# Kernel optimization log

Hardware: AMD Instinct MI355X
Metric: run time of the kernel (lower is better)

The kernel has to match this reference:

```python
import jax, jax.numpy as jnp
import numpy as np
import math
from itertools import combinations_with_replacement

M_MODES = 10      # photonic modes
N_PHOT = 5        # photons in input state [1,0,1,0,...]
HIDDEN = 100      # number of px phase shifters (hidden_dim)
IN_DIM = 784
N_CLASSES = 10
BATCH = 128

# Fock output states with bunching: multisets of N_PHOT modes -> C(14,5)=2002
_STATES = np.array(list(combinations_with_replacement(range(M_MODES), N_PHOT)), dtype=np.int32)  # [S, n] row indices
_FACT = np.array([
    np.prod([math.factorial(int(c)) for c in np.bincount(s, minlength=M_MODES)])
    for s in _STATES
], dtype=np.float32)  # prod t_j! per output state
# Input-state mode columns (occupied modes) and factorial product (=1 since all occupancies are 1)
_IN_COLS = np.array([0, 2, 4, 6, 8], dtype=np.int32)
# Ryser subsets over n=5 rows
_BITS = np.array([[(k >> i) & 1 for i in range(N_PHOT)] for k in range(2 ** N_PHOT)], dtype=np.float32)  # [K, n]
_SIGNS = ((-1.0) ** (N_PHOT - _BITS.sum(axis=1))).astype(np.float32)  # (-1)^n * (-1)^{|S|}


def _rand_unitary(rng, m):
    z = rng.standard_normal((m, m)) + 1j * rng.standard_normal((m, m))
    q, r = np.linalg.qr(z)
    q = q * (np.diag(r) / np.abs(np.diag(r)))
    return q.astype(np.complex64)


def setup_inputs() -> dict:
    rng = np.random.default_rng(0)
    x = jnp.asarray(rng.standard_normal((BATCH, IN_DIM)), dtype=jnp.float32)
    W1 = jnp.asarray(rng.standard_normal((HIDDEN, IN_DIM)) * 0.03, dtype=jnp.float32)
    b1 = jnp.zeros((HIDDEN,), dtype=jnp.float32)
    UL = _rand_unitary(rng, M_MODES)
    UR = _rand_unitary(rng, M_MODES)
    S = _STATES.shape[0]
    W2 = jnp.asarray(rng.standard_normal((N_CLASSES, S)) * 0.02, dtype=jnp.float32)
    b2 = jnp.zeros((N_CLASSES,), dtype=jnp.float32)
    return {
        "x": x, "W1": W1, "b1": b1,
        "wl_re": jnp.asarray(UL.real), "wl_im": jnp.asarray(UL.imag),
        "wr_re": jnp.asarray(UR.real), "wr_im": jnp.asarray(UR.imag),
        "W2": W2, "b2": b2,
    }


def _forward(x, W1, b1, wl_re, wl_im, wr_re, wr_im, W2, b2):
    B = x.shape[0]
    # downscaling linear + sigmoid -> phase-shifter values px in (0,1)
    h = jax.nn.sigmoid(x @ W1.T + b1)  # [B, HIDDEN]
    # phase shifter i sits on mode i % m; commuting phases on a mode sum
    theta = h.reshape(B, HIDDEN // M_MODES, M_MODES).sum(axis=1)  # [B, m]
    WL = (wl_re + 1j * wl_im).astype(jnp.complex64)
    WR = (wr_re + 1j * wr_im).astype(jnp.complex64)
    phase = jnp.exp(1j * theta.astype(jnp.complex64))  # [B, m]
    # total unitary U = WR @ diag(phase) @ WL
    U = jnp.einsum('pq,bq,qr->bpr', WR, phase, WL)  # [B, m, m]
    A = U[:, :, _IN_COLS]  # columns for occupied input modes -> [B, m, n]
    # per output Fock state, take rows (with multiplicity) -> [B, S, n, n]
    Mx = A[:, jnp.asarray(_STATES), :]
    masks = jnp.asarray(_BITS)   # [K, n]
    signs = jnp.asarray(_SIGNS)  # [K]
    # Ryser: perm = (-1)^n sum_S (-1)^{|S|} prod_j (sum_{i in S} M[i,j])
    rs = jnp.einsum('kn,bsnj->bskj', masks, Mx)       # [B, S, K, n]
    p = jnp.prod(rs, axis=-1)                          # [B, S, K]
    perm = jnp.einsum('k,bsk->bs', signs, p)           # [B, S] complex
    amp = perm / jnp.sqrt(jnp.asarray(_FACT))
    prob = amp.real ** 2 + amp.imag ** 2               # boson-sampling output distribution [B, S]
    return prob @ W2.T + b2                            # output Linear [B, N_CLASSES]


def reference(x, W1, b1, wl_re, wl_im, wr_re, wr_im, W2, b2):
    return _forward(x, W1, b1, wl_re, wl_im, wr_re, wr_im, W2, b2)
```

## Files before the change

### kernel.cpp

```cpp
#include <hip/hip_runtime.h>
#include <utility>
#include <math.h>

#define BATCH     128
#define IN_DIM    784
#define HIDDEN    100
#define MM        10
#define NPH       5
#define NSTATES   2002
#define NCLASSES  10

struct StateTbl { unsigned v[NSTATES]; };

constexpr StateTbl make_state_tbl() {
    StateTbl t{};
    int idx = 0;
    for (int a = 0; a < MM; ++a)
    for (int b = a; b < MM; ++b)
    for (int c = b; c < MM; ++c)
    for (int d = c; d < MM; ++d)
    for (int e = d; e < MM; ++e) {
        int cnt[MM] = {};
        cnt[a]++; cnt[b]++; cnt[c]++; cnt[d]++; cnt[e]++;
        int f = 1;
        for (int m = 0; m < MM; ++m) {
            int kf = 1;
            for (int i = 2; i <= cnt[m]; ++i) kf *= i;
            f *= kf;
        }
        t.v[idx++] = (unsigned)a | ((unsigned)b << 4) | ((unsigned)c << 8) |
                     ((unsigned)d << 12) | ((unsigned)e << 16) |
                     ((unsigned)f << 20);
    }
    return t;
}

__device__ const StateTbl STATE_TBL = make_state_tbl();

__global__ __launch_bounds__(256) void qc_stageA(
    const float* __restrict__ x, const float* __restrict__ W1,
    const float* __restrict__ b1,
    const float* __restrict__ wl_re, const float* __restrict__ wl_im,
    const float* __restrict__ wr_re, const float* __restrict__ wr_im,
    const float* __restrict__ b2,
    float* __restrict__ A_ws, float* __restrict__ out)
{
    __shared__ __align__(16) float xs[IN_DIM];
    __shared__ float part[200];
    __shared__ float hs[HIDDEN];
    __shared__ float phc[MM], phs_[MM];
    __shared__ float plr[50], pli[50];

    const int b   = blockIdx.x;
    const int tid = threadIdx.x;

    for (int i = tid; i < IN_DIM; i += 256) xs[i] = x[b * IN_DIM + i];
    if (tid < NCLASSES) out[b * NCLASSES + tid] = b2[tid];
    __syncthreads();

    if (tid < 200) {
        const int j = tid >> 1, half = tid & 1;
        const float* wr_ = W1 + j * IN_DIM + half * 392;
        const float* xr  = xs + half * 392;
        float4 acc = make_float4(0.f, 0.f, 0.f, 0.f);
        #pragma unroll 4
        for (int i = 0; i < 392; i += 4) {
            float4 w  = *(const float4*)(wr_ + i);
            float4 xv = *(const float4*)(xr + i);
            acc.x += w.x * xv.x; acc.y += w.y * xv.y;
            acc.z += w.z * xv.z; acc.w += w.w * xv.w;
        }
        part[tid] = (acc.x + acc.y) + (acc.z + acc.w);
    }
    __syncthreads();

    if (tid < HIDDEN) {
        float t = part[2 * tid] + part[2 * tid + 1] + b1[tid];
        hs[tid] = 1.0f / (1.0f + expf(-t));
    }
    __syncthreads();

    if (tid < MM) {
        float th = 0.f;
        #pragma unroll
        for (int g = 0; g < MM; ++g) th += hs[g * MM + tid];
        float sv, cv;
        sincosf(th, &sv, &cv);
        phc[tid] = cv; phs_[tid] = sv;
    }
    __syncthreads();

    if (tid < 50) {
        const int q = tid / 5, c = tid % 5;
        const float lr = wl_re[q * MM + 2 * c], li = wl_im[q * MM + 2 * c];
        plr[tid] = phc[q] * lr - phs_[q] * li;
        pli[tid] = phc[q] * li + phs_[q] * lr;
    }
    __syncthreads();

    if (tid < 50) {
        const int p = tid / 5, c = tid % 5;
        float ar = 0.f, ai = 0.f;
        #pragma unroll
        for (int q = 0; q < MM; ++q) {
            const float rr = wr_re[p * MM + q], ri = wr_im[p * MM + q];
            const float br = plr[q * 5 + c],    bi = pli[q * 5 + c];
            ar += rr * br - ri * bi;
            ai += rr * bi + ri * br;
        }
        A_ws[(b * 50 + tid) * 2 + 0] = ar;
        A_ws[(b * 50 + tid) * 2 + 1] = ai;
    }
}

template <int K>
__device__ __forceinline__ void ryser_step(
    const float (&mr)[5][5], const float (&mi)[5][5],
    float (&cr)[5], float (&ci)[5], float& accr, float& acci)
{
    constexpr int  bit  = (K & 1) ? 0 : ((K & 2) ? 1 : ((K & 4) ? 2 : ((K & 8) ? 3 : 4)));
    constexpr int  gray = K ^ (K >> 1);
    constexpr bool addf = ((gray >> bit) & 1) != 0;
    constexpr int  pc   = ((gray) & 1) + ((gray >> 1) & 1) + ((gray >> 2) & 1) +
                          ((gray >> 3) & 1) + ((gray >> 4) & 1);
    #pragma unroll
    for (int j = 0; j < 5; ++j) {
        if (addf) { cr[j] += mr[bit][j]; ci[j] += mi[bit][j]; }
        else      { cr[j] -= mr[bit][j]; ci[j] -= mi[bit][j]; }
    }
    float pr = cr[0], pi = ci[0];
    #pragma unroll
    for (int j = 1; j < 5; ++j) {
        const float nr = pr * cr[j] - pi * ci[j];
        const float ni = pr * ci[j] + pi * cr[j];
        pr = nr; pi = ni;
    }
    if constexpr (((NPH - pc) & 1) != 0) { accr -= pr; acci -= pi; }
    else                                 { accr += pr; acci += pi; }
}

template <int... Ks>
__device__ __forceinline__ void ryser_run(
    std::integer_sequence<int, Ks...>,
    const float (&mr)[5][5], const float (&mi)[5][5],
    float (&cr)[5], float (&ci)[5], float& accr, float& acci)
{
    (ryser_step<Ks + 1>(mr, mi, cr, ci, accr, acci), ...);
}

__global__ __launch_bounds__(256) void qc_stageB(
    const float* __restrict__ A_ws, const float* __restrict__ W2,
    float* __restrict__ out)
{
    __shared__ float2 a2[50];
    __shared__ float  wsum[4][NCLASSES];

    const int tid = threadIdx.x;
    const int b   = blockIdx.x >> 3;
    const int s   = ((blockIdx.x & 7) << 8) + tid;

    if (tid < 50) a2[tid] = ((const float2*)A_ws)[b * 50 + tid];
    __syncthreads();

    const bool valid = (s < NSTATES);
    float prob = 0.f;

    if (valid) {
        const unsigned w = STATE_TBL.v[s];

        float mr[5][5], mi[5][5];
        #pragma unroll
        for (int n = 0; n < 5; ++n) {
            const int base = ((w >> (4 * n)) & 15) * 5;
            #pragma unroll
            for (int j = 0; j < 5; ++j) {
                const float2 e = a2[base + j];
                mr[n][j] = e.x; mi[n][j] = e.y;
            }
        }

        float cr[5] = {0,0,0,0,0}, ci[5] = {0,0,0,0,0};
        float accr = 0.f, acci = 0.f;
        ryser_run(std::make_integer_sequence<int, 31>{}, mr, mi, cr, ci, accr, acci);

        const float fact = (float)(w >> 20);
        prob = (accr * accr + acci * acci) / fact;
    }

    #pragma unroll
    for (int c = 0; c < NCLASSES; ++c) {
        float v = 0.f;
        if (valid) v = prob * W2[c * NSTATES + s];
        #pragma unroll
        for (int off = 32; off > 0; off >>= 1) v += __shfl_down(v, off, 64);
        if ((tid & 63) == 0) wsum[tid >> 6][c] = v;
    }
    __syncthreads();
    if (tid < NCLASSES) {
        const float t = (wsum[0][tid] + wsum[1][tid]) + (wsum[2][tid] + wsum[3][tid]);
        atomicAdd(out + b * NCLASSES + tid, t);
    }
}

extern "C" void kernel_launch(void* const* d_in, const int* in_sizes, int n_in,
                              void* d_out, int out_size, void* d_ws, size_t ws_size,
                              hipStream_t stream)
{
    const float* x     = (const float*)d_in[0];
    const float* W1    = (const float*)d_in[1];
    const float* b1    = (const float*)d_in[2];
    const float* wl_re = (const float*)d_in[3];
    const float* wl_im = (const float*)d_in[4];
    const float* wr_re = (const float*)d_in[5];
    const float* wr_im = (const float*)d_in[6];
    const float* W2    = (const float*)d_in[7];
    const float* b2    = (const float*)d_in[8];
    float*       out   = (float*)d_out;
    float*       A_ws  = (float*)d_ws;

    qc_stageA<<<BATCH, 256, 0, stream>>>(x, W1, b1, wl_re, wl_im,
                                         wr_re, wr_im, b2, A_ws, out);
    qc_stageB<<<BATCH * 8, 256, 0, stream>>>(A_ws, W2, out);
}
```

Measured before the change: 101.0 us.

## Switch permanent computation from Ryser to Glynn Gray-code formula, two states per thread

New measurement: 95.47 us. 5.5% less time.

```diff
diff --git a/kernel.cpp b/kernel.cpp
--- a/kernel.cpp
+++ b/kernel.cpp
@@ -114,19 +114,20 @@
 }
 
 template <int K>
-__device__ __forceinline__ void ryser_step(
+__device__ __forceinline__ void glynn_step(
     const float (&mr)[5][5], const float (&mi)[5][5],
     float (&cr)[5], float (&ci)[5], float& accr, float& acci)
 {
-    constexpr int  bit  = (K & 1) ? 0 : ((K & 2) ? 1 : ((K & 4) ? 2 : ((K & 8) ? 3 : 4)));
-    constexpr int  gray = K ^ (K >> 1);
-    constexpr bool addf = ((gray >> bit) & 1) != 0;
-    constexpr int  pc   = ((gray) & 1) + ((gray >> 1) & 1) + ((gray >> 2) & 1) +
-                          ((gray >> 3) & 1) + ((gray >> 4) & 1);
+    constexpr int   bit  = (K & 1) ? 0 : ((K & 2) ? 1 : ((K & 4) ? 2 : 3));
+    constexpr int   gray = K ^ (K >> 1);
+    constexpr int   row  = bit + 1;
+    constexpr float s2   = ((gray >> bit) & 1) ? -2.0f : 2.0f;
+    constexpr int   pc   = (gray & 1) + ((gray >> 1) & 1) +
+                           ((gray >> 2) & 1) + ((gray >> 3) & 1);
     #pragma unroll
     for (int j = 0; j < 5; ++j) {
-        if (addf) { cr[j] += mr[bit][j]; ci[j] += mi[bit][j]; }
-        else      { cr[j] -= mr[bit][j]; ci[j] -= mi[bit][j]; }
+        cr[j] = fmaf(s2, mr[row][j], cr[j]);
+        ci[j] = fmaf(s2, mi[row][j], ci[j]);
     }
     float pr = cr[0], pi = ci[0];
     #pragma unroll
@@ -135,17 +136,17 @@
         const float ni = pr * ci[j] + pi * cr[j];
         pr = nr; pi = ni;
     }
-    if constexpr (((NPH - pc) & 1) != 0) { accr -= pr; acci -= pi; }
-    else                                 { accr += pr; acci += pi; }
+    if constexpr ((pc & 1) != 0) { accr -= pr; acci -= pi; }
+    else                         { accr += pr; acci += pi; }
 }
 
 template <int... Ks>
-__device__ __forceinline__ void ryser_run(
+__device__ __forceinline__ void glynn_run(
     std::integer_sequence<int, Ks...>,
     const float (&mr)[5][5], const float (&mi)[5][5],
     float (&cr)[5], float (&ci)[5], float& accr, float& acci)
 {
-    (ryser_step<Ks + 1>(mr, mi, cr, ci, accr, acci), ...);
+    (glynn_step<Ks + 1>(mr, mi, cr, ci, accr, acci), ...);
 }
 
 __global__ __launch_bounds__(256) void qc_stageB(
@@ -155,42 +156,63 @@
     __shared__ float2 a2[50];
     __shared__ float  wsum[4][NCLASSES];
 
-    const int tid = threadIdx.x;
-    const int b   = blockIdx.x >> 3;
-    const int s   = ((blockIdx.x & 7) << 8) + tid;
+    const int tid   = threadIdx.x;
+    const int b     = blockIdx.x >> 2;
+    const int sbase = (blockIdx.x & 3) << 9;
 
     if (tid < 50) a2[tid] = ((const float2*)A_ws)[b * 50 + tid];
     __syncthreads();
 
-    const bool valid = (s < NSTATES);
-    float prob = 0.f;
-
-    if (valid) {
-        const unsigned w = STATE_TBL.v[s];
-
-        float mr[5][5], mi[5][5];
-        #pragma unroll
-        for (int n = 0; n < 5; ++n) {
-            const int base = ((w >> (4 * n)) & 15) * 5;
+    float cls[NCLASSES] = {0,0,0,0,0,0,0,0,0,0};
+
+    #pragma unroll
+    for (int t = 0; t < 2; ++t) {
+        const int s = sbase + (t << 8) + tid;
+        if (s < NSTATES) {
+            const unsigned w = STATE_TBL.v[s];
+
+            float mr[5][5], mi[5][5];
+            #pragma unroll
+            for (int n = 0; n < 5; ++n) {
+                const int base = ((w >> (4 * n)) & 15) * 5;
+                #pragma unroll
+                for (int j = 0; j < 5; ++j) {
+                    const float2 e = a2[base + j];
+                    mr[n][j] = e.x; mi[n][j] = e.y;
+                }
+            }
+
+            float cr[5], ci[5];
             #pragma unroll
             for (int j = 0; j < 5; ++j) {
-                const float2 e = a2[base + j];
-                mr[n][j] = e.x; mi[n][j] = e.y;
+                cr[j] = ((mr[0][j] + mr[1][j]) + (mr[2][j] + mr[3][j])) + mr[4][j];
+                ci[j] = ((mi[0][j] + mi[1][j]) + (mi[2][j] + mi[3][j])) + mi[4][j];
             }
-        }
-
-        float cr[5] = {0,0,0,0,0}, ci[5] = {0,0,0,0,0};
-        float accr = 0.f, acci = 0.f;
-        ryser_run(std::make_integer_sequence<int, 31>{}, mr, mi, cr, ci, accr, acci);
-
-        const float fact = (float)(w >> 20);
-        prob = (accr * accr + acci * acci) / fact;
+            float accr = 0.f, acci = 0.f;
+            {
+                float pr = cr[0], pi = ci[0];
+                #pragma unroll
+                for (int j = 1; j < 5; ++j) {
+                    const float nr = pr * cr[j] - pi * ci[j];
+                    const float ni = pr * ci[j] + pi * cr[j];
+                    pr = nr; pi = ni;
+                }
+                accr = pr; acci = pi;
+            }
+            glynn_run(std::make_integer_sequence<int, 15>{}, mr, mi, cr, ci, accr, acci);
+
+            const float fact = (float)(w >> 20);
+            const float prob = (accr * accr + acci * acci) / (256.0f * fact);
+
+            #pragma unroll
+            for (int c = 0; c < NCLASSES; ++c)
+                cls[c] = fmaf(prob, W2[c * NSTATES + s], cls[c]);
+        }
     }
 
     #pragma unroll
     for (int c = 0; c < NCLASSES; ++c) {
-        float v = 0.f;
-        if (valid) v = prob * W2[c * NSTATES + s];
+        float v = cls[c];
         #pragma unroll
         for (int off = 32; off > 0; off >>= 1) v += __shfl_down(v, off, 64);
         if ((tid & 63) == 0) wsum[tid >> 6][c] = v;
@@ -220,5 +242,5 @@
 
     qc_stageA<<<BATCH, 256, 0, stream>>>(x, W1, b1, wl_re, wl_im,
                                          wr_re, wr_im, b2, A_ws, out);
-    qc_stageB<<<BATCH * 8, 256, 0, stream>>>(A_ws, W2, out);
-}
+    qc_stageB<<<BATCH * 4, 256, 0, stream>>>(A_ws, W2, out);
+}
```
